# Kernel optimization log

Measured on AMD Instinct MI355X. Metric: run time of the kernel, lower is better.

The kernel has to match this reference:

```python
import jax, jax.numpy as jnp
import numpy as np

E, D, H, T = 64, 512, 1024, 256  # num_experts, dim, hidden_dim, tokens


def setup_inputs() -> dict:
    key = jax.random.key(0)
    k1, k2, k3, k4 = jax.random.split(key, 4)
    x = jax.random.normal(k1, (T, D), dtype=jnp.float32)
    expert_idx = jax.random.randint(k2, (T,), 0, E, dtype=jnp.int64)
    # kaiming_uniform-ish init scale for the batched expert weights
    fc1_w = jax.random.normal(k3, (E, H, D), dtype=jnp.float32) * 0.02  # [E, hidden, dim]
    fc2_w = jax.random.normal(k4, (E, D, H), dtype=jnp.float32) * 0.02  # [E, dim, hidden]
    return {"x": x, "expert_idx": expert_idx, "fc1_w": fc1_w, "fc2_w": fc2_w}


def reference(x, expert_idx, fc1_w, fc2_w):
    # Gather full expert weight matrices per token (faithful to torch module),
    # then per-token matvec: out = silu(x @ W1^T) @ W2^T
    w1 = fc1_w[expert_idx]                      # [T, H, D]
    w2 = fc2_w[expert_idx]                      # [T, D, H]
    h = jax.nn.silu(jnp.einsum('td,thd->th', x, w1))  # [T, H]
    out = jnp.einsum('th,tdh->td', h, w2)             # [T, D]
    return out
```

## Files before the change

kernel.cpp:

```cpp
#include <hip/hip_runtime.h>
#include <math.h>

#define NE 64
#define ND 512
#define NH 1024
#define NT 256
#define NC 8

__device__ __forceinline__ int build_group(const int* __restrict__ idx, int e,
                                           int* tok_lds, int* wsum) {
    const int t = threadIdx.x, wave = t >> 6, lane = t & 63;
    const bool m = (idx[t] == e);
    const unsigned long long mask = __ballot(m);
    if (lane == 0) wsum[wave] = __popcll(mask);
    __syncthreads();
    int before = 0;
#pragma unroll
    for (int w = 0; w < 3; ++w) before += (w < wave) ? wsum[w] : 0;
    const int nt = wsum[0] + wsum[1] + wsum[2] + wsum[3];
    if (m) {
        int pos = before + __popcll(mask & ((1ull << lane) - 1ull));
        tok_lds[pos] = t;
    }
    __syncthreads();
    if (nt > 0 && t >= nt && t < nt + NC) tok_lds[t] = tok_lds[0];
    __syncthreads();
    return nt;
}

__device__ __forceinline__ float fused_reduce8(float v[NC], int lane) {
#pragma unroll
    for (int i = 0; i < 4; ++i) {
        float lo = v[i], hi = v[i + 4];
        float send = (lane & 1) ? lo : hi;
        float recv = __shfl_xor(send, 1);
        v[i] = ((lane & 1) ? hi : lo) + recv;
    }
#pragma unroll
    for (int i = 0; i < 2; ++i) {
        float lo = v[i], hi = v[i + 2];
        float send = (lane & 2) ? lo : hi;
        float recv = __shfl_xor(send, 2);
        v[i] = ((lane & 2) ? hi : lo) + recv;
    }
    {
        float lo = v[0], hi = v[1];
        float send = (lane & 4) ? lo : hi;
        float recv = __shfl_xor(send, 4);
        v[0] = ((lane & 4) ? hi : lo) + recv;
    }
    v[0] += __shfl_xor(v[0], 8);
    v[0] += __shfl_xor(v[0], 16);
    v[0] += __shfl_xor(v[0], 32);
    return v[0];
}

__global__ __launch_bounds__(256) void fc1_kernel(
    const float* __restrict__ x, const float* __restrict__ w1,
    const int* __restrict__ idx, float* __restrict__ h) {
    __shared__ int tok_lds[NT + NC];
    __shared__ int wsum[4];
    const int e  = blockIdx.x >> 4;
    const int ch = blockIdx.x & 15;
    const int tid = threadIdx.x, wave = tid >> 6, lane = tid & 63;
    const int nt = build_group(idx, e, tok_lds, wsum);
    if (nt == 0) return;
    const float* w1e = w1 + (size_t)e * NH * ND;
    const int j0 = ch * 64 + wave * 16;

    for (int base = 0; base < nt; base += NC) {
        float4 xa[NC], xb[NC];
#pragma unroll
        for (int t = 0; t < NC; ++t) {
            const float* xr = x + (size_t)tok_lds[base + t] * ND;
            xa[t] = *(const float4*)(xr + lane * 4);
            xb[t] = *(const float4*)(xr + 256 + lane * 4);
        }
#pragma unroll 4
        for (int r = 0; r < 16; ++r) {
            const float* wr = w1e + (size_t)(j0 + r) * ND;
            const float4 wa = *(const float4*)(wr + lane * 4);
            const float4 wb = *(const float4*)(wr + 256 + lane * 4);
            float acc[NC];
#pragma unroll
            for (int t = 0; t < NC; ++t) {
                acc[t] = wa.x * xa[t].x + wa.y * xa[t].y + wa.z * xa[t].z + wa.w * xa[t].w
                       + wb.x * xb[t].x + wb.y * xb[t].y + wb.z * xb[t].z + wb.w * xb[t].w;
            }
            float p = fused_reduce8(acc, lane);
            if (lane < NC) {
                int t = ((lane & 1) << 2) | (lane & 2) | ((lane >> 2) & 1);
                if (base + t < nt) {
                    int tk = tok_lds[base + t];
                    float s = p / (1.0f + __expf(-p));
                    h[(size_t)tk * NH + (j0 + r)] = s;
                }
            }
        }
    }
}

__global__ __launch_bounds__(256) void fc2_kernel(
    const float* __restrict__ h, const float* __restrict__ w2,
    const int* __restrict__ idx, float* __restrict__ out) {
    __shared__ int tok_lds[NT + NC];
    __shared__ int wsum[4];
    const int e  = blockIdx.x >> 4;
    const int ch = blockIdx.x & 15;
    const int tid = threadIdx.x, wave = tid >> 6, lane = tid & 63;
    const int nt = build_group(idx, e, tok_lds, wsum);
    if (nt == 0) return;
    const float* w2e = w2 + (size_t)e * ND * NH;
    const int d0 = ch * 32 + wave * 8;

    for (int base = 0; base < nt; base += NC) {
        float4 hb0[NC], hb1[NC], hb2[NC], hb3[NC];
#pragma unroll
        for (int t = 0; t < NC; ++t) {
            const float* hr = h + (size_t)tok_lds[base + t] * NH;
            hb0[t] = *(const float4*)(hr + lane * 4);
            hb1[t] = *(const float4*)(hr + 256 + lane * 4);
            hb2[t] = *(const float4*)(hr + 512 + lane * 4);
            hb3[t] = *(const float4*)(hr + 768 + lane * 4);
        }
#pragma unroll 2
        for (int r = 0; r < 8; ++r) {
            const float* wr = w2e + (size_t)(d0 + r) * NH;
            const float4 w0 = *(const float4*)(wr + lane * 4);
            const float4 w1v = *(const float4*)(wr + 256 + lane * 4);
            const float4 w2v = *(const float4*)(wr + 512 + lane * 4);
            const float4 w3v = *(const float4*)(wr + 768 + lane * 4);
            float acc[NC];
#pragma unroll
            for (int t = 0; t < NC; ++t) {
                acc[t] = w0.x * hb0[t].x + w0.y * hb0[t].y + w0.z * hb0[t].z + w0.w * hb0[t].w
                       + w1v.x * hb1[t].x + w1v.y * hb1[t].y + w1v.z * hb1[t].z + w1v.w * hb1[t].w
                       + w2v.x * hb2[t].x + w2v.y * hb2[t].y + w2v.z * hb2[t].z + w2v.w * hb2[t].w
                       + w3v.x * hb3[t].x + w3v.y * hb3[t].y + w3v.z * hb3[t].z + w3v.w * hb3[t].w;
            }
            float p = fused_reduce8(acc, lane);
            if (lane < NC) {
                int t = ((lane & 1) << 2) | (lane & 2) | ((lane >> 2) & 1);
                if (base + t < nt) {
                    int tk = tok_lds[base + t];
                    out[(size_t)tk * ND + (d0 + r)] = p;
                }
            }
        }
    }
}

extern "C" void kernel_launch(void* const* d_in, const int* in_sizes, int n_in,
                              void* d_out, int out_size, void* d_ws, size_t ws_size,
                              hipStream_t stream) {
    const float* x    = (const float*)d_in[0];
    const int*   eidx = (const int*)d_in[1];
    const float* fc1w = (const float*)d_in[2];
    const float* fc2w = (const float*)d_in[3];
    float* out = (float*)d_out;
    float* h   = (float*)d_ws;

    fc1_kernel<<<NE * 16, 256, 0, stream>>>(x, fc1w, eidx, h);
    fc2_kernel<<<NE * 16, 256, 0, stream>>>(h, fc2w, eidx, out);
}
```

Before: 70.03 us.

## Fuse fc1 and fc2 per hidden-chunk with partial sums and a reduction kernel

Merges the two expert matvec kernels into one: each block computes a 64-wide slice of the hidden activation into LDS, then immediately multiplies it by the matching column slice of fc2 weights, writing per-chunk partial outputs. A small second kernel sums the 16 partials per output element. This removes the global round trip of h and the dependency between the two kernels, but adds a 16x partial buffer (8 MB of writes and reads) plus narrower, strided fc2 weight loads.

```diff
diff --git a/kernel.cpp b/kernel.cpp
--- a/kernel.cpp
+++ b/kernel.cpp
@@ -6,6 +6,9 @@
 #define NH 1024
 #define NT 256
 #define NC 8
+#define NCH 16
+#define CHROWS (NH/NCH)
+
 
 __device__ __forceinline__ int build_group(const int* __restrict__ idx, int e,
                                            int* tok_lds, int* wsum) {
@@ -28,7 +31,7 @@
     return nt;
 }
 
-__device__ __forceinline__ float fused_reduce8(float v[NC], int lane) {
+__device__ __forceinline__ float fused_reduce_16(float v[NC], int lane) {
 #pragma unroll
     for (int i = 0; i < 4; ++i) {
         float lo = v[i], hi = v[i + 4];
@@ -50,23 +53,34 @@
         v[0] = ((lane & 4) ? hi : lo) + recv;
     }
     v[0] += __shfl_xor(v[0], 8);
-    v[0] += __shfl_xor(v[0], 16);
-    v[0] += __shfl_xor(v[0], 32);
     return v[0];
 }
 
-__global__ __launch_bounds__(256) void fc1_kernel(
+__device__ __forceinline__ float fused_reduce_64(float v[NC], int lane) {
+    float p = fused_reduce_16(v, lane);
+    p += __shfl_xor(p, 16);
+    p += __shfl_xor(p, 32);
+    return p;
+}
+
+__global__ __launch_bounds__(256) void moe_fused_kernel(
     const float* __restrict__ x, const float* __restrict__ w1,
-    const int* __restrict__ idx, float* __restrict__ h) {
+    const float* __restrict__ w2, const int* __restrict__ idx,
+    float* __restrict__ partial) {
     __shared__ int tok_lds[NT + NC];
     __shared__ int wsum[4];
+    __shared__ float hs[NC][CHROWS];
+
     const int e  = blockIdx.x >> 4;
     const int ch = blockIdx.x & 15;
     const int tid = threadIdx.x, wave = tid >> 6, lane = tid & 63;
     const int nt = build_group(idx, e, tok_lds, wsum);
     if (nt == 0) return;
+
     const float* w1e = w1 + (size_t)e * NH * ND;
-    const int j0 = ch * 64 + wave * 16;
+    const float* w2e = w2 + (size_t)e * ND * NH;
+    const int j0 = ch * CHROWS;
+    const int jw = j0 + wave * 16;
 
     for (int base = 0; base < nt; base += NC) {
         float4 xa[NC], xb[NC];
@@ -78,7 +92,7 @@
         }
 #pragma unroll 4
         for (int r = 0; r < 16; ++r) {
-            const float* wr = w1e + (size_t)(j0 + r) * ND;
+            const float* wr = w1e + (size_t)(jw + r) * ND;
             const float4 wa = *(const float4*)(wr + lane * 4);
             const float4 wb = *(const float4*)(wr + 256 + lane * 4);
             float acc[NC];
@@ -87,67 +101,53 @@
                 acc[t] = wa.x * xa[t].x + wa.y * xa[t].y + wa.z * xa[t].z + wa.w * xa[t].w
                        + wb.x * xb[t].x + wb.y * xb[t].y + wb.z * xb[t].z + wb.w * xb[t].w;
             }
-            float p = fused_reduce8(acc, lane);
+            float p = fused_reduce_64(acc, lane);
             if (lane < NC) {
+                int t = ((lane & 1) << 2) | (lane & 2) | ((lane >> 2) & 1);
+                hs[t][wave * 16 + r] = p / (1.0f + __expf(-p));
+            }
+        }
+        __syncthreads();
+
+        float4 hf[NC];
+#pragma unroll
+        for (int t = 0; t < NC; ++t)
+            hf[t] = *(const float4*)&hs[t][(lane & 15) * 4];
+
+        const int dw = wave * 128 + (lane >> 4);
+#pragma unroll 4
+        for (int it = 0; it < 32; ++it) {
+            const int d = dw + it * 4;
+            const float4 wv = *(const float4*)(w2e + (size_t)d * NH + j0 + (lane & 15) * 4);
+            float acc[NC];
+#pragma unroll
+            for (int t = 0; t < NC; ++t) {
+                acc[t] = wv.x * hf[t].x + wv.y * hf[t].y + wv.z * hf[t].z + wv.w * hf[t].w;
+            }
+            float p = fused_reduce_16(acc, lane);
+            if ((lane & 8) == 0) {
                 int t = ((lane & 1) << 2) | (lane & 2) | ((lane >> 2) & 1);
                 if (base + t < nt) {
                     int tk = tok_lds[base + t];
-                    float s = p / (1.0f + __expf(-p));
-                    h[(size_t)tk * NH + (j0 + r)] = s;
+                    partial[((size_t)ch * NT + tk) * ND + d] = p;
                 }
             }
         }
+        __syncthreads();
     }
 }
 
-__global__ __launch_bounds__(256) void fc2_kernel(
-    const float* __restrict__ h, const float* __restrict__ w2,
-    const int* __restrict__ idx, float* __restrict__ out) {
-    __shared__ int tok_lds[NT + NC];
-    __shared__ int wsum[4];
-    const int e  = blockIdx.x >> 4;
-    const int ch = blockIdx.x & 15;
-    const int tid = threadIdx.x, wave = tid >> 6, lane = tid & 63;
-    const int nt = build_group(idx, e, tok_lds, wsum);
-    if (nt == 0) return;
-    const float* w2e = w2 + (size_t)e * ND * NH;
-    const int d0 = ch * 32 + wave * 8;
-
-    for (int base = 0; base < nt; base += NC) {
-        float4 hb0[NC], hb1[NC], hb2[NC], hb3[NC];
+__global__ __launch_bounds__(256) void sum_kernel(
+    const float* __restrict__ partial, float* __restrict__ out) {
+    const int i = blockIdx.x * 256 + threadIdx.x;
+    const float4* p = (const float4*)partial;
+    float4 s = p[i];
 #pragma unroll
-        for (int t = 0; t < NC; ++t) {
-            const float* hr = h + (size_t)tok_lds[base + t] * NH;
-            hb0[t] = *(const float4*)(hr + lane * 4);
-            hb1[t] = *(const float4*)(hr + 256 + lane * 4);
-            hb2[t] = *(const float4*)(hr + 512 + lane * 4);
-            hb3[t] = *(const float4*)(hr + 768 + lane * 4);
-        }
-#pragma unroll 2
-        for (int r = 0; r < 8; ++r) {
-            const float* wr = w2e + (size_t)(d0 + r) * NH;
-            const float4 w0 = *(const float4*)(wr + lane * 4);
-            const float4 w1v = *(const float4*)(wr + 256 + lane * 4);
-            const float4 w2v = *(const float4*)(wr + 512 + lane * 4);
-            const float4 w3v = *(const float4*)(wr + 768 + lane * 4);
-            float acc[NC];
-#pragma unroll
-            for (int t = 0; t < NC; ++t) {
-                acc[t] = w0.x * hb0[t].x + w0.y * hb0[t].y + w0.z * hb0[t].z + w0.w * hb0[t].w
-                       + w1v.x * hb1[t].x + w1v.y * hb1[t].y + w1v.z * hb1[t].z + w1v.w * hb1[t].w
-                       + w2v.x * hb2[t].x + w2v.y * hb2[t].y + w2v.z * hb2[t].z + w2v.w * hb2[t].w
-                       + w3v.x * hb3[t].x + w3v.y * hb3[t].y + w3v.z * hb3[t].z + w3v.w * hb3[t].w;
-            }
-            float p = fused_reduce8(acc, lane);
-            if (lane < NC) {
-                int t = ((lane & 1) << 2) | (lane & 2) | ((lane >> 2) & 1);
-                if (base + t < nt) {
-                    int tk = tok_lds[base + t];
-                    out[(size_t)tk * ND + (d0 + r)] = p;
-                }
-            }
-        }
+    for (int c = 1; c < NCH; ++c) {
+        float4 v = p[(size_t)c * (NT * ND / 4) + i];
+        s.x += v.x; s.y += v.y; s.z += v.z; s.w += v.w;
     }
+    ((float4*)out)[i] = s;
 }
 
 extern "C" void kernel_launch(void* const* d_in, const int* in_sizes, int n_in,
@@ -157,9 +157,9 @@
     const int*   eidx = (const int*)d_in[1];
     const float* fc1w = (const float*)d_in[2];
     const float* fc2w = (const float*)d_in[3];
-    float* out = (float*)d_out;
-    float* h   = (float*)d_ws;
+    float* out     = (float*)d_out;
+    float* partial = (float*)d_ws;
 
-    fc1_kernel<<<NE * 16, 256, 0, stream>>>(x, fc1w, eidx, h);
-    fc2_kernel<<<NE * 16, 256, 0, stream>>>(h, fc2w, eidx, out);
+    moe_fused_kernel<<<NE * NCH, 256, 0, stream>>>(x, fc1w, fc2w, eidx, partial);
+    sum_kernel<<<(NT * ND / 4) / 256, 256, 0, stream>>>(partial, out);
 }
```

Result: slower. 81.79 us (+16.8%).

## Double grid size and split fc2 token groups across wave pairs

Applied to the files above, without the earlier changes.

Both kernels now launch 32 blocks per expert instead of 16, halving the rows each wave handles so more blocks are available to fill the GPU's compute units. In fc2, wave pairs split each 8-token group into two halves of 4 tokens, using a new 4-way shuffle reduction. This cuts the registers needed for h buffers and raises parallelism, at the cost of reloading each weight row twice per token group and repeating the token-grouping setup in more blocks.

```diff
diff --git a/kernel.cpp b/kernel.cpp
--- a/kernel.cpp
+++ b/kernel.cpp
@@ -6,6 +6,7 @@
 #define NH 1024
 #define NT 256
 #define NC 8
+
 
 __device__ __forceinline__ int build_group(const int* __restrict__ idx, int e,
                                            int* tok_lds, int* wsum) {
@@ -28,7 +29,7 @@
     return nt;
 }
 
-__device__ __forceinline__ float fused_reduce8(float v[NC], int lane) {
+__device__ __forceinline__ float fused_reduce8_64(float v[NC], int lane) {
 #pragma unroll
     for (int i = 0; i < 4; ++i) {
         float lo = v[i], hi = v[i + 4];
@@ -55,18 +56,39 @@
     return v[0];
 }
 
+__device__ __forceinline__ float fused_reduce4_64(float v[4], int lane) {
+#pragma unroll
+    for (int i = 0; i < 2; ++i) {
+        float lo = v[i], hi = v[i + 2];
+        float send = (lane & 1) ? lo : hi;
+        float recv = __shfl_xor(send, 1);
+        v[i] = ((lane & 1) ? hi : lo) + recv;
+    }
+    {
+        float lo = v[0], hi = v[1];
+        float send = (lane & 2) ? lo : hi;
+        float recv = __shfl_xor(send, 2);
+        v[0] = ((lane & 2) ? hi : lo) + recv;
+    }
+    v[0] += __shfl_xor(v[0], 4);
+    v[0] += __shfl_xor(v[0], 8);
+    v[0] += __shfl_xor(v[0], 16);
+    v[0] += __shfl_xor(v[0], 32);
+    return v[0];
+}
+
 __global__ __launch_bounds__(256) void fc1_kernel(
     const float* __restrict__ x, const float* __restrict__ w1,
     const int* __restrict__ idx, float* __restrict__ h) {
     __shared__ int tok_lds[NT + NC];
     __shared__ int wsum[4];
-    const int e  = blockIdx.x >> 4;
-    const int ch = blockIdx.x & 15;
+    const int e  = blockIdx.x >> 5;
+    const int ch = blockIdx.x & 31;
     const int tid = threadIdx.x, wave = tid >> 6, lane = tid & 63;
     const int nt = build_group(idx, e, tok_lds, wsum);
     if (nt == 0) return;
     const float* w1e = w1 + (size_t)e * NH * ND;
-    const int j0 = ch * 64 + wave * 16;
+    const int jw = ch * 32 + wave * 8;
 
     for (int base = 0; base < nt; base += NC) {
         float4 xa[NC], xb[NC];
@@ -77,8 +99,8 @@
             xb[t] = *(const float4*)(xr + 256 + lane * 4);
         }
 #pragma unroll 4
-        for (int r = 0; r < 16; ++r) {
-            const float* wr = w1e + (size_t)(j0 + r) * ND;
+        for (int r = 0; r < 8; ++r) {
+            const float* wr = w1e + (size_t)(jw + r) * ND;
             const float4 wa = *(const float4*)(wr + lane * 4);
             const float4 wb = *(const float4*)(wr + 256 + lane * 4);
             float acc[NC];
@@ -87,13 +109,13 @@
                 acc[t] = wa.x * xa[t].x + wa.y * xa[t].y + wa.z * xa[t].z + wa.w * xa[t].w
                        + wb.x * xb[t].x + wb.y * xb[t].y + wb.z * xb[t].z + wb.w * xb[t].w;
             }
-            float p = fused_reduce8(acc, lane);
+            float p = fused_reduce8_64(acc, lane);
             if (lane < NC) {
                 int t = ((lane & 1) << 2) | (lane & 2) | ((lane >> 2) & 1);
                 if (base + t < nt) {
                     int tk = tok_lds[base + t];
                     float s = p / (1.0f + __expf(-p));
-                    h[(size_t)tk * NH + (j0 + r)] = s;
+                    h[(size_t)tk * NH + (jw + r)] = s;
                 }
             }
         }
@@ -105,44 +127,47 @@
     const int* __restrict__ idx, float* __restrict__ out) {
     __shared__ int tok_lds[NT + NC];
     __shared__ int wsum[4];
-    const int e  = blockIdx.x >> 4;
-    const int ch = blockIdx.x & 15;
+    const int e  = blockIdx.x >> 5;
+    const int ch = blockIdx.x & 31;
     const int tid = threadIdx.x, wave = tid >> 6, lane = tid & 63;
     const int nt = build_group(idx, e, tok_lds, wsum);
     if (nt == 0) return;
     const float* w2e = w2 + (size_t)e * ND * NH;
-    const int d0 = ch * 32 + wave * 8;
+    const int tokhalf = wave >> 1;
+    const int d0 = ch * 16 + (wave & 1) * 8;
 
     for (int base = 0; base < nt; base += NC) {
-        float4 hb0[NC], hb1[NC], hb2[NC], hb3[NC];
+        if (base + tokhalf * 4 >= nt) break;
+        float4 hb0[4], hb1[4], hb2[4], hb3[4];
 #pragma unroll
-        for (int t = 0; t < NC; ++t) {
-            const float* hr = h + (size_t)tok_lds[base + t] * NH;
+        for (int t = 0; t < 4; ++t) {
+            const float* hr = h + (size_t)tok_lds[base + tokhalf * 4 + t] * NH;
             hb0[t] = *(const float4*)(hr + lane * 4);
             hb1[t] = *(const float4*)(hr + 256 + lane * 4);
             hb2[t] = *(const float4*)(hr + 512 + lane * 4);
             hb3[t] = *(const float4*)(hr + 768 + lane * 4);
         }
-#pragma unroll 2
+#pragma unroll 4
         for (int r = 0; r < 8; ++r) {
             const float* wr = w2e + (size_t)(d0 + r) * NH;
             const float4 w0 = *(const float4*)(wr + lane * 4);
             const float4 w1v = *(const float4*)(wr + 256 + lane * 4);
             const float4 w2v = *(const float4*)(wr + 512 + lane * 4);
             const float4 w3v = *(const float4*)(wr + 768 + lane * 4);
-            float acc[NC];
+            float acc[4];
 #pragma unroll
-            for (int t = 0; t < NC; ++t) {
+            for (int t = 0; t < 4; ++t) {
                 acc[t] = w0.x * hb0[t].x + w0.y * hb0[t].y + w0.z * hb0[t].z + w0.w * hb0[t].w
                        + w1v.x * hb1[t].x + w1v.y * hb1[t].y + w1v.z * hb1[t].z + w1v.w * hb1[t].w
                        + w2v.x * hb2[t].x + w2v.y * hb2[t].y + w2v.z * hb2[t].z + w2v.w * hb2[t].w
                        + w3v.x * hb3[t].x + w3v.y * hb3[t].y + w3v.z * hb3[t].z + w3v.w * hb3[t].w;
             }
-            float p = fused_reduce8(acc, lane);
-            if (lane < NC) {
-                int t = ((lane & 1) << 2) | (lane & 2) | ((lane >> 2) & 1);
-                if (base + t < nt) {
-                    int tk = tok_lds[base + t];
+            float p = fused_reduce4_64(acc, lane);
+            if (lane < 4) {
+                int t = ((lane & 1) << 1) | ((lane >> 1) & 1);
+                int slot = base + tokhalf * 4 + t;
+                if (slot < nt) {
+                    int tk = tok_lds[slot];
                     out[(size_t)tk * ND + (d0 + r)] = p;
                 }
             }
@@ -160,6 +185,6 @@
     float* out = (float*)d_out;
     float* h   = (float*)d_ws;
 
-    fc1_kernel<<<NE * 16, 256, 0, stream>>>(x, fc1w, eidx, h);
-    fc2_kernel<<<NE * 16, 256, 0, stream>>>(h, fc2w, eidx, out);
+    fc1_kernel<<<NE * 32, 256, 0, stream>>>(x, fc1w, eidx, h);
+    fc2_kernel<<<NE * 32, 256, 0, stream>>>(h, fc2w, eidx, out);
 }
```

Measured after the change: 61.19 us. -12.6%, faster.
